# Performance work log

Hardware: AMD Instinct MI355X
Metric: run time of the kernel (lower is better)

Reference implementation:

```python
import jax, jax.numpy as jnp
import numpy as np

COMMITMENT_COST = 0.25

def setup_inputs() -> dict:
    key = jax.random.key(0)
    k1, k2 = jax.random.split(key)
    inputs = jax.random.normal(k1, (32, 64, 64, 64), dtype=jnp.float32)  # NCHW, C == embedding_dim
    num_embeddings, embedding_dim = 512, 64
    # nn.Embedding weight init: uniform(-1/num_embeddings, 1/num_embeddings)
    weight = jax.random.uniform(k2, (num_embeddings, embedding_dim), dtype=jnp.float32,
                                minval=-1.0 / num_embeddings, maxval=1.0 / num_embeddings)
    return {"inputs": inputs, "weight": weight}

def reference(inputs, weight):
    B, C, H, W = inputs.shape
    K, D = weight.shape
    # permute to NHWC then flatten tokens: [B*H*W, D]
    flat = jnp.transpose(inputs, (0, 2, 3, 1)).reshape(-1, D)
    # squared L2 distances to each codebook vector: [N, K]
    distances = (jnp.sum(flat * flat, axis=1, keepdims=True)
                 - 2.0 * flat @ weight.T
                 + jnp.sum(weight * weight, axis=1))
    encoding_indices = jnp.argmin(distances, axis=1)  # [N]
    # direct gather instead of one-hot matmul (same math)
    # NOTE: original code views flat (NHWC-ordered) rows back into the NCHW
    # input shape WITHOUT inverse-permuting -- replicated faithfully here.
    quantized = weight[encoding_indices].reshape(inputs.shape)
    e_latent_loss = jnp.mean((jax.lax.stop_gradient(quantized) - inputs) ** 2)
    q_latent_loss = jnp.mean((quantized - jax.lax.stop_gradient(inputs)) ** 2)
    loss = q_latent_loss + COMMITMENT_COST * e_latent_loss
    # straight-through estimator
    quantized_st = inputs + jax.lax.stop_gradient(quantized - inputs)
    # perplexity via index counts (equivalent to mean of one-hot encodings)
    N = flat.shape[0]
    counts = jnp.zeros((K,), dtype=flat.dtype).at[encoding_indices].add(1.0)
    avg_probs = counts / N
    perplexity = jnp.exp(-jnp.sum(avg_probs * jnp.log(avg_probs + 1e-10)))
    return quantized_st, loss, perplexity
```

## Files before the change

kernel.cpp:

```cpp
#include <hip/hip_runtime.h>
#include <math.h>


#define NTOK 131072
#define KCODES 512
#define HW 4096
#define CHW 262144
#define NELEM 8388608

typedef __attribute__((ext_vector_type(8))) short short8;
typedef __attribute__((ext_vector_type(4))) float f32x4;

static __device__ __forceinline__ unsigned short f2bf(float f) {
    unsigned u = __float_as_uint(f);
    unsigned r = u + 0x7FFFu + ((u >> 16) & 1u);
    return (unsigned short)(r >> 16);
}

__global__ __launch_bounds__(512, 4) void vq_main(const float* __restrict__ in,
                                                  const float* __restrict__ w,
                                                  float* __restrict__ out,
                                                  float* __restrict__ pcounts,
                                                  double* __restrict__ ssep,
                                                  float* __restrict__ counts,
                                                  double* __restrict__ sse_acc,
                                                  const int amode) {
    __shared__ unsigned short wh[KCODES * 64];
    __shared__ float wsqp[KCODES];
    __shared__ int idxbuf[256];
    __shared__ int hist[KCODES];
    __shared__ double sred[8];

    const int tid = threadIdx.x;
    const int lane = tid & 63, wv = tid >> 6;
    const int col = lane & 15, quad = lane >> 4;
    const int ntok0 = blockIdx.x * 256;

    wsqp[tid] = 1.25f;
    hist[tid] = 0;
    __syncthreads();

    const float* gbase = in + (ntok0 >> 12) * CHW + (ntok0 & 4095) + wv * 32 + col;
    short8 ah[2][2];
    float xsq = 0.f;
#pragma unroll
    for (int it = 0; it < 8; ++it) {
        const int g = it * 512 + tid;
        const int cc = g & 15, qd = (g >> 4) & 3, ch = (g >> 6) & 1, tt = g >> 7;
        const float4* src = (const float4*)(w + (tt * 16 + cc) * 64 + ch * 32 + qd * 8);
        const float4 v0 = src[0], v1 = src[1];
        const int sub = it >> 2, c = (it >> 1) & 1, j0 = (it & 1) * 4;
        const float* gp = gbase + sub * 16 + (c * 32 + quad * 8 + j0) * HW;
        const float x0 = gp[0 * HW], x1 = gp[1 * HW], x2 = gp[2 * HW], x3 = gp[3 * HW];

        short8 hv;
        hv[0] = (short)f2bf(v0.x); hv[1] = (short)f2bf(v0.y);
        hv[2] = (short)f2bf(v0.z); hv[3] = (short)f2bf(v0.w);
        hv[4] = (short)f2bf(v1.x); hv[5] = (short)f2bf(v1.y);
        hv[6] = (short)f2bf(v1.z); hv[7] = (short)f2bf(v1.w);
        *(short8*)(wh + g * 8) = hv;
        float ws2 = v0.x * v0.x;
        ws2 = fmaf(v0.y, v0.y, ws2); ws2 = fmaf(v0.z, v0.z, ws2);
        ws2 = fmaf(v0.w, v0.w, ws2); ws2 = fmaf(v1.x, v1.x, ws2);
        ws2 = fmaf(v1.y, v1.y, ws2); ws2 = fmaf(v1.z, v1.z, ws2);
        ws2 = fmaf(v1.w, v1.w, ws2);
        atomicAdd(&wsqp[tt * 16 + cc], ws2);

        ah[sub][c][j0 + 0] = (short)f2bf(-2.0f * x0);
        ah[sub][c][j0 + 1] = (short)f2bf(-2.0f * x1);
        ah[sub][c][j0 + 2] = (short)f2bf(-2.0f * x2);
        ah[sub][c][j0 + 3] = (short)f2bf(-2.0f * x3);
        xsq = fmaf(x0, x0, xsq); xsq = fmaf(x1, x1, xsq);
        xsq = fmaf(x2, x2, xsq); xsq = fmaf(x3, x3, xsq);
    }
    __syncthreads();

    unsigned runkey[2][4];
#pragma unroll
    for (int sub = 0; sub < 2; ++sub)
#pragma unroll
        for (int r = 0; r < 4; ++r) runkey[sub][r] = 0xFFFFFFFFu;

#pragma unroll 1
    for (int t = 0; t < 32; ++t) {
        const unsigned short* ph = wh + t * 1024 + quad * 128 + col * 8;
        const short8 b0 = *(const short8*)ph;
        const short8 b1 = *(const short8*)(ph + 512);
        const int code = t * 16 + col;
        const float seed = wsqp[code];
#pragma unroll
        for (int sub = 0; sub < 2; ++sub) {
            f32x4 acc = {seed, seed, seed, seed};
            acc = __builtin_amdgcn_mfma_f32_16x16x32_bf16(ah[sub][0], b0, acc, 0, 0, 0);
            acc = __builtin_amdgcn_mfma_f32_16x16x32_bf16(ah[sub][1], b1, acc, 0, 0, 0);
#pragma unroll
            for (int r = 0; r < 4; ++r) {
                const unsigned key = (__float_as_uint(acc[r]) << 9) | code;
                runkey[sub][r] = key < runkey[sub][r] ? key : runkey[sub][r];
            }
        }
    }

#pragma unroll
    for (int s = 1; s < 16; s <<= 1)
#pragma unroll
        for (int sub = 0; sub < 2; ++sub)
#pragma unroll
            for (int r = 0; r < 4; ++r) {
                const unsigned o = __shfl_xor(runkey[sub][r], s, 64);
                runkey[sub][r] = o < runkey[sub][r] ? o : runkey[sub][r];
            }

    float dsum = 0.f;
    if (col == 0) {
#pragma unroll
        for (int sub = 0; sub < 2; ++sub)
#pragma unroll
            for (int r = 0; r < 4; ++r) {
                const unsigned key = runkey[sub][r];
                idxbuf[wv * 32 + sub * 16 + quad * 4 + r] = (int)(key & 511u);
                dsum += __uint_as_float((key >> 9) | 0x3F800000u) - 1.25f;
            }
    }
    float contrib = xsq + dsum;
#pragma unroll
    for (int off = 32; off > 0; off >>= 1) contrib += __shfl_down(contrib, off, 64);
    if (lane == 0) sred[wv] = (double)contrib;
    __syncthreads();

    if (tid < 256) atomicAdd(&hist[idxbuf[tid]], 1);

#pragma unroll
    for (int p = 0; p < 2; ++p) {
        const int tl = p * 16 + (lane >> 2), q = lane & 3;
        const int n = ntok0 + wv * 32 + tl;
        const int bidx = idxbuf[wv * 32 + tl];
        const float4* wr = (const float4*)(w + bidx * 64 + q * 16);
        float4* op = (float4*)(out + n * 64 + q * 16);
#pragma unroll
        for (int i = 0; i < 4; ++i) op[i] = wr[i];
    }
    __syncthreads();

    if (!amode) {
        pcounts[(blockIdx.x << 9) + tid] = (float)hist[tid];
        if (tid == 0) {
            double s = sred[0];
#pragma unroll
            for (int i = 1; i < 8; ++i) s += sred[i];
            ssep[blockIdx.x] = s;
        }
    } else {
        const int h = hist[tid];
        if (h) atomicAdd(&counts[tid], (float)h);
        if (tid == 0) {
            double s = sred[0];
#pragma unroll
            for (int i = 1; i < 8; ++i) s += sred[i];
            atomicAdd(sse_acc, s);
        }
    }
}

__global__ __launch_bounds__(512) void vq_final_p(const float* __restrict__ pcounts,
                                                  const double* __restrict__ ssep,
                                                  float* __restrict__ out) {
    __shared__ float part[4][512];
    __shared__ double red[512];
    __shared__ double sred[512];
    const int t = threadIdx.x;
    const int q = t >> 7, c4 = (t & 127) << 2;

    const float4* base = (const float4*)pcounts + (q << 14) + (c4 >> 2);
    float4 s = {0.f, 0.f, 0.f, 0.f};
#pragma unroll 16
    for (int b = 0; b < 128; ++b) {
        const float4 v = base[b << 7];
        s.x += v.x; s.y += v.y; s.z += v.z; s.w += v.w;
    }
    *(float4*)&part[q][c4] = s;
    sred[t] = ssep[t];
    __syncthreads();

    const float cnt = part[0][t] + part[1][t] + part[2][t] + part[3][t];
    const double p = (double)cnt / (double)NTOK;
    red[t] = p * log(p + 1e-10);
    __syncthreads();
#pragma unroll
    for (int st = 256; st > 0; st >>= 1) {
        if (t < st) { red[t] += red[t + st]; sred[t] += sred[t + st]; }
        __syncthreads();
    }
    if (t == 0) {
        out[NELEM] = (float)((sred[0] / (double)NELEM) * 1.25);
        out[NELEM + 1] = (float)exp(-red[0]);
    }
}

__global__ __launch_bounds__(512) void vq_final_a(const float* __restrict__ counts,
                                                  const double* __restrict__ sse_acc,
                                                  float* __restrict__ out) {
    __shared__ double red[512];
    const int k = threadIdx.x;
    const double p = (double)counts[k] / (double)NTOK;
    red[k] = p * log(p + 1e-10);
    __syncthreads();
#pragma unroll
    for (int st = 256; st > 0; st >>= 1) {
        if (k < st) red[k] += red[k + st];
        __syncthreads();
    }
    if (k == 0) {
        out[NELEM] = (float)((*sse_acc / (double)NELEM) * 1.25);
        out[NELEM + 1] = (float)exp(-red[0]);
    }
}

extern "C" void kernel_launch(void* const* d_in, const int* in_sizes, int n_in,
                              void* d_out, int out_size, void* d_ws, size_t ws_size,
                              hipStream_t stream) {
    const float* in = (const float*)d_in[0];
    const float* w = (const float*)d_in[1];
    float* out = (float*)d_out;
    char* ws = (char*)d_ws;

    const size_t need = (size_t)512 * 512 * 4 + 512 * 8;
    if (ws_size >= need) {
        float* pcounts = (float*)ws;
        double* ssep = (double*)(ws + (size_t)512 * 512 * 4);
        vq_main<<<512, 512, 0, stream>>>(in, w, out, pcounts, ssep,
                                         nullptr, nullptr, 0);
        vq_final_p<<<1, 512, 0, stream>>>(pcounts, ssep, out);
    } else {
        float* counts = (float*)ws;
        double* sse_acc = (double*)(ws + 2048);
        hipMemsetAsync(ws, 0, 2056, stream);
        vq_main<<<512, 512, 0, stream>>>(in, w, out, nullptr, nullptr,
                                         counts, sse_acc, 1);
        vq_final_a<<<1, 512, 0, stream>>>(counts, sse_acc, out);
    }
}
```

Baseline: 117.4 us.

## Fuse final reduction into main kernel via last-block counters and nontemporal stores

Drops the separate final reduction kernel. Each block takes a ticket from a global atomic counter, and the last 16 blocks spin until all 512 blocks have finished. Those 16 then reduce slices of the per-block histograms, and a second counter picks one block to compute loss and perplexity. The histogram atomics also no longer wait on a block barrier, and the quantized output is written with nontemporal stores. This saves a kernel launch and the tail serialization, but adds a memset of the counters and spin-waiting that relies on all blocks being co-resident or otherwise making progress.

New measurement: 172.1 us. +46.6%, slower.

```diff
diff --git a/kernel.cpp b/kernel.cpp
--- a/kernel.cpp
+++ b/kernel.cpp
@@ -22,14 +22,17 @@
                                                   float* __restrict__ out,
                                                   float* __restrict__ pcounts,
                                                   double* __restrict__ ssep,
+                                                  float* __restrict__ part2,
+                                                  unsigned* __restrict__ ctrs,
                                                   float* __restrict__ counts,
                                                   double* __restrict__ sse_acc,
                                                   const int amode) {
-    __shared__ unsigned short wh[KCODES * 64];
+    __shared__ __align__(16) unsigned short wh[KCODES * 64];
     __shared__ float wsqp[KCODES];
     __shared__ int idxbuf[256];
     __shared__ int hist[KCODES];
     __shared__ double sred[8];
+    __shared__ int role_sh;
 
     const int tid = threadIdx.x;
     const int lane = tid & 63, wv = tid >> 6;
@@ -126,19 +129,21 @@
 #pragma unroll
     for (int off = 32; off > 0; off >>= 1) contrib += __shfl_down(contrib, off, 64);
     if (lane == 0) sred[wv] = (double)contrib;
-    __syncthreads();
-
-    if (tid < 256) atomicAdd(&hist[idxbuf[tid]], 1);
+
+    if (lane < 32) atomicAdd(&hist[idxbuf[wv * 32 + lane]], 1);
 
 #pragma unroll
     for (int p = 0; p < 2; ++p) {
         const int tl = p * 16 + (lane >> 2), q = lane & 3;
         const int n = ntok0 + wv * 32 + tl;
         const int bidx = idxbuf[wv * 32 + tl];
-        const float4* wr = (const float4*)(w + bidx * 64 + q * 16);
-        float4* op = (float4*)(out + n * 64 + q * 16);
-#pragma unroll
-        for (int i = 0; i < 4; ++i) op[i] = wr[i];
+        const f32x4* wr = (const f32x4*)(w + bidx * 64 + q * 16);
+        f32x4* op = (f32x4*)(out + n * 64 + q * 16);
+#pragma unroll
+        for (int i = 0; i < 4; ++i) {
+            const f32x4 v = wr[i];
+            __builtin_nontemporal_store(v, op + i);
+        }
     }
     __syncthreads();
 
@@ -149,6 +154,61 @@
 #pragma unroll
             for (int i = 1; i < 8; ++i) s += sred[i];
             ssep[blockIdx.x] = s;
+        }
+        __syncthreads();
+        if (tid == 0) {
+            __threadfence();
+            role_sh = (int)atomicAdd(ctrs, 1u);
+        }
+        __syncthreads();
+        const int old = role_sh;
+
+        if (old >= 512 - 16) {
+            const int r = old - (512 - 16);
+            if (tid == 0) {
+                while (__hip_atomic_load(ctrs, __ATOMIC_RELAXED,
+                                         __HIP_MEMORY_SCOPE_AGENT) < 512u)
+                    __builtin_amdgcn_s_sleep(2);
+            }
+            __syncthreads();
+            __threadfence();
+
+            const float* pc = pcounts + (r << 14) + tid;
+            float s = 0.f;
+#pragma unroll
+            for (int b = 0; b < 32; ++b) s += pc[b << 9];
+            part2[(r << 9) + tid] = s;
+            __syncthreads();
+            if (tid == 0) {
+                __threadfence();
+                role_sh = (int)atomicAdd(ctrs + 1, 1u);
+            }
+            __syncthreads();
+
+            if (role_sh == 15) {
+                __threadfence();
+                double* const dred = (double*)wh;
+                double* const dsred = dred + KCODES;
+                float cnt = 0.f;
+#pragma unroll
+                for (int rr = 0; rr < 16; ++rr) cnt += part2[(rr << 9) + tid];
+                const double p = (double)cnt / (double)NTOK;
+                dred[tid] = p * log(p + 1e-10);
+                dsred[tid] = ssep[tid];
+                __syncthreads();
+#pragma unroll
+                for (int st = 256; st > 0; st >>= 1) {
+                    if (tid < st) {
+                        dred[tid] += dred[tid + st];
+                        dsred[tid] += dsred[tid + st];
+                    }
+                    __syncthreads();
+                }
+                if (tid == 0) {
+                    out[NELEM] = (float)((dsred[0] / (double)NELEM) * 1.25);
+                    out[NELEM + 1] = (float)exp(-dred[0]);
+                }
+            }
         }
     } else {
         const int h = hist[tid];
@@ -159,41 +219,6 @@
             for (int i = 1; i < 8; ++i) s += sred[i];
             atomicAdd(sse_acc, s);
         }
-    }
-}
-
-__global__ __launch_bounds__(512) void vq_final_p(const float* __restrict__ pcounts,
-                                                  const double* __restrict__ ssep,
-                                                  float* __restrict__ out) {
-    __shared__ float part[4][512];
-    __shared__ double red[512];
-    __shared__ double sred[512];
-    const int t = threadIdx.x;
-    const int q = t >> 7, c4 = (t & 127) << 2;
-
-    const float4* base = (const float4*)pcounts + (q << 14) + (c4 >> 2);
-    float4 s = {0.f, 0.f, 0.f, 0.f};
-#pragma unroll 16
-    for (int b = 0; b < 128; ++b) {
-        const float4 v = base[b << 7];
-        s.x += v.x; s.y += v.y; s.z += v.z; s.w += v.w;
-    }
-    *(float4*)&part[q][c4] = s;
-    sred[t] = ssep[t];
-    __syncthreads();
-
-    const float cnt = part[0][t] + part[1][t] + part[2][t] + part[3][t];
-    const double p = (double)cnt / (double)NTOK;
-    red[t] = p * log(p + 1e-10);
-    __syncthreads();
-#pragma unroll
-    for (int st = 256; st > 0; st >>= 1) {
-        if (t < st) { red[t] += red[t + st]; sred[t] += sred[t + st]; }
-        __syncthreads();
-    }
-    if (t == 0) {
-        out[NELEM] = (float)((sred[0] / (double)NELEM) * 1.25);
-        out[NELEM + 1] = (float)exp(-red[0]);
     }
 }
 
@@ -224,19 +249,25 @@
     float* out = (float*)d_out;
     char* ws = (char*)d_ws;
 
-    const size_t need = (size_t)512 * 512 * 4 + 512 * 8;
+    const size_t PC = 0;
+    const size_t SS = (size_t)1 << 20;
+    const size_t P2 = SS + 4096;
+    const size_t CT = P2 + 32768;
+    const size_t need = CT + 8;
     if (ws_size >= need) {
-        float* pcounts = (float*)ws;
-        double* ssep = (double*)(ws + (size_t)512 * 512 * 4);
-        vq_main<<<512, 512, 0, stream>>>(in, w, out, pcounts, ssep,
+        float* pcounts = (float*)(ws + PC);
+        double* ssep = (double*)(ws + SS);
+        float* part2 = (float*)(ws + P2);
+        unsigned* ctrs = (unsigned*)(ws + CT);
+        (void)hipMemsetAsync(ctrs, 0, 8, stream);
+        vq_main<<<512, 512, 0, stream>>>(in, w, out, pcounts, ssep, part2, ctrs,
                                          nullptr, nullptr, 0);
-        vq_final_p<<<1, 512, 0, stream>>>(pcounts, ssep, out);
     } else {
         float* counts = (float*)ws;
         double* sse_acc = (double*)(ws + 2048);
-        hipMemsetAsync(ws, 0, 2056, stream);
-        vq_main<<<512, 512, 0, stream>>>(in, w, out, nullptr, nullptr,
-                                         counts, sse_acc, 1);
+        (void)hipMemsetAsync(ws, 0, 2056, stream);
+        vq_main<<<512, 512, 0, stream>>>(in, w, out, nullptr, nullptr, nullptr,
+                                         nullptr, counts, sse_acc, 1);
         vq_final_a<<<1, 512, 0, stream>>>(counts, sse_acc, out);
     }
 }
```

## Halve per-block tokens, stage codebook in two LDS halves, use byte partial counts

Applied to the files above, without the earlier changes.

Each block now handles 128 tokens instead of 256, launching 1024 blocks, and the bf16 codebook is staged through LDS in two 256-code halves. This halves LDS use (32KB to 16KB) and register state per block, allowing a higher occupancy hint of 8 waves-per-EU, so more blocks run concurrently to hide input-load latency. The trade is an extra barrier and a second conversion pass per block, and each block converts the codebook on twice as many blocks overall. Per-block histograms are written as bytes and unpacked in the final kernel, shrinking partial-count traffic, and the final reduction now sums two SSE partials per thread.

After: 126.6 us. 1.08x slower.

```diff
diff --git a/kernel.cpp b/kernel.cpp
--- a/kernel.cpp
+++ b/kernel.cpp
@@ -17,40 +17,41 @@
     return (unsigned short)(r >> 16);
 }
 
-__global__ __launch_bounds__(512, 4) void vq_main(const float* __restrict__ in,
+__global__ __launch_bounds__(512, 8) void vq_main(const float* __restrict__ in,
                                                   const float* __restrict__ w,
                                                   float* __restrict__ out,
-                                                  float* __restrict__ pcounts,
+                                                  unsigned char* __restrict__ pcounts,
                                                   double* __restrict__ ssep,
                                                   float* __restrict__ counts,
                                                   double* __restrict__ sse_acc,
                                                   const int amode) {
-    __shared__ unsigned short wh[KCODES * 64];
+    __shared__ __align__(16) unsigned short wh[256 * 64];
     __shared__ float wsqp[KCODES];
-    __shared__ int idxbuf[256];
+    __shared__ int idxbuf[128];
     __shared__ int hist[KCODES];
     __shared__ double sred[8];
 
     const int tid = threadIdx.x;
     const int lane = tid & 63, wv = tid >> 6;
     const int col = lane & 15, quad = lane >> 4;
-    const int ntok0 = blockIdx.x * 256;
+    const int ntok0 = blockIdx.x * 128;
 
     wsqp[tid] = 1.25f;
     hist[tid] = 0;
     __syncthreads();
 
-    const float* gbase = in + (ntok0 >> 12) * CHW + (ntok0 & 4095) + wv * 32 + col;
-    short8 ah[2][2];
+    const float* gbase = in + (ntok0 >> 12) * CHW + (ntok0 & 4095) + wv * 16 + col;
+    short8 ah[2];
     float xsq = 0.f;
 #pragma unroll
-    for (int it = 0; it < 8; ++it) {
+    for (int it = 0; it < 4; ++it) {
         const int g = it * 512 + tid;
         const int cc = g & 15, qd = (g >> 4) & 3, ch = (g >> 6) & 1, tt = g >> 7;
-        const float4* src = (const float4*)(w + (tt * 16 + cc) * 64 + ch * 32 + qd * 8);
+        const int code = tt * 16 + cc;
+        const float4* src = (const float4*)(w + code * 64 + ch * 32 + qd * 8);
         const float4 v0 = src[0], v1 = src[1];
-        const int sub = it >> 2, c = (it >> 1) & 1, j0 = (it & 1) * 4;
-        const float* gp = gbase + sub * 16 + (c * 32 + quad * 8 + j0) * HW;
+        const int c = it >> 1, j0 = (it & 1) * 4;
+        const float* gp = gbase + (c * 32 + quad * 8 + j0) * HW;
         const float x0 = gp[0 * HW], x1 = gp[1 * HW], x2 = gp[2 * HW], x3 = gp[3 * HW];
 
         short8 hv;
@@ -64,77 +65,106 @@
         ws2 = fmaf(v0.w, v0.w, ws2); ws2 = fmaf(v1.x, v1.x, ws2);
         ws2 = fmaf(v1.y, v1.y, ws2); ws2 = fmaf(v1.z, v1.z, ws2);
         ws2 = fmaf(v1.w, v1.w, ws2);
-        atomicAdd(&wsqp[tt * 16 + cc], ws2);
-
-        ah[sub][c][j0 + 0] = (short)f2bf(-2.0f * x0);
-        ah[sub][c][j0 + 1] = (short)f2bf(-2.0f * x1);
-        ah[sub][c][j0 + 2] = (short)f2bf(-2.0f * x2);
-        ah[sub][c][j0 + 3] = (short)f2bf(-2.0f * x3);
+        atomicAdd(&wsqp[code], ws2);
+
+        ah[c][j0 + 0] = (short)f2bf(-2.0f * x0);
+        ah[c][j0 + 1] = (short)f2bf(-2.0f * x1);
+        ah[c][j0 + 2] = (short)f2bf(-2.0f * x2);
+        ah[c][j0 + 3] = (short)f2bf(-2.0f * x3);
         xsq = fmaf(x0, x0, xsq); xsq = fmaf(x1, x1, xsq);
         xsq = fmaf(x2, x2, xsq); xsq = fmaf(x3, x3, xsq);
     }
     __syncthreads();
 
-    unsigned runkey[2][4];
-#pragma unroll
-    for (int sub = 0; sub < 2; ++sub)
-#pragma unroll
-        for (int r = 0; r < 4; ++r) runkey[sub][r] = 0xFFFFFFFFu;
+    unsigned runkey[4];
+#pragma unroll
+    for (int r = 0; r < 4; ++r) runkey[r] = 0xFFFFFFFFu;
 
 #pragma unroll 1
-    for (int t = 0; t < 32; ++t) {
+    for (int t = 0; t < 16; ++t) {
         const unsigned short* ph = wh + t * 1024 + quad * 128 + col * 8;
         const short8 b0 = *(const short8*)ph;
         const short8 b1 = *(const short8*)(ph + 512);
         const int code = t * 16 + col;
         const float seed = wsqp[code];
-#pragma unroll
-        for (int sub = 0; sub < 2; ++sub) {
-            f32x4 acc = {seed, seed, seed, seed};
-            acc = __builtin_amdgcn_mfma_f32_16x16x32_bf16(ah[sub][0], b0, acc, 0, 0, 0);
-            acc = __builtin_amdgcn_mfma_f32_16x16x32_bf16(ah[sub][1], b1, acc, 0, 0, 0);
-#pragma unroll
-            for (int r = 0; r < 4; ++r) {
-                const unsigned key = (__float_as_uint(acc[r]) << 9) | code;
-                runkey[sub][r] = key < runkey[sub][r] ? key : runkey[sub][r];
-            }
+        f32x4 acc = {seed, seed, seed, seed};
+        acc = __builtin_amdgcn_mfma_f32_16x16x32_bf16(ah[0], b0, acc, 0, 0, 0);
+        acc = __builtin_amdgcn_mfma_f32_16x16x32_bf16(ah[1], b1, acc, 0, 0, 0);
+#pragma unroll
+        for (int r = 0; r < 4; ++r) {
+            const unsigned key = (__float_as_uint(acc[r]) << 9) | code;
+            runkey[r] = key < runkey[r] ? key : runkey[r];
+        }
+    }
+    __syncthreads();
+
+#pragma unroll
+    for (int it = 0; it < 4; ++it) {
+        const int g = it * 512 + tid;
+        const int cc = g & 15, qd = (g >> 4) & 3, ch = (g >> 6) & 1, tt = g >> 7;
+        const int code = 256 + tt * 16 + cc;
+        const float4* src = (const float4*)(w + code * 64 + ch * 32 + qd * 8);
+        const float4 v0 = src[0], v1 = src[1];
+        short8 hv;
+        hv[0] = (short)f2bf(v0.x); hv[1] = (short)f2bf(v0.y);
+        hv[2] = (short)f2bf(v0.z); hv[3] = (short)f2bf(v0.w);
+        hv[4] = (short)f2bf(v1.x); hv[5] = (short)f2bf(v1.y);
+        hv[6] = (short)f2bf(v1.z); hv[7] = (short)f2bf(v1.w);
+        *(short8*)(wh + g * 8) = hv;
+        float ws2 = v0.x * v0.x;
+        ws2 = fmaf(v0.y, v0.y, ws2); ws2 = fmaf(v0.z, v0.z, ws2);
+        ws2 = fmaf(v0.w, v0.w, ws2); ws2 = fmaf(v1.x, v1.x, ws2);
+        ws2 = fmaf(v1.y, v1.y, ws2); ws2 = fmaf(v1.z, v1.z, ws2);
+        ws2 = fmaf(v1.w, v1.w, ws2);
+        atomicAdd(&wsqp[code], ws2);
+    }
+    __syncthreads();
+
+#pragma unroll 1
+    for (int t = 0; t < 16; ++t) {
+        const unsigned short* ph = wh + t * 1024 + quad * 128 + col * 8;
+        const short8 b0 = *(const short8*)ph;
+        const short8 b1 = *(const short8*)(ph + 512);
+        const int code = 256 + t * 16 + col;
+        const float seed = wsqp[code];
+        f32x4 acc = {seed, seed, seed, seed};
+        acc = __builtin_amdgcn_mfma_f32_16x16x32_bf16(ah[0], b0, acc, 0, 0, 0);
+        acc = __builtin_amdgcn_mfma_f32_16x16x32_bf16(ah[1], b1, acc, 0, 0, 0);
+#pragma unroll
+        for (int r = 0; r < 4; ++r) {
+            const unsigned key = (__float_as_uint(acc[r]) << 9) | code;
+            runkey[r] = key < runkey[r] ? key : runkey[r];
         }
     }
 
 #pragma unroll
     for (int s = 1; s < 16; s <<= 1)
 #pragma unroll
-        for (int sub = 0; sub < 2; ++sub)
-#pragma unroll
-            for (int r = 0; r < 4; ++r) {
-                const unsigned o = __shfl_xor(runkey[sub][r], s, 64);
-                runkey[sub][r] = o < runkey[sub][r] ? o : runkey[sub][r];
-            }
+        for (int r = 0; r < 4; ++r) {
+            const unsigned o = __shfl_xor(runkey[r], s, 64);
+            runkey[r] = o < runkey[r] ? o : runkey[r];
+        }
 
     float dsum = 0.f;
     if (col == 0) {
 #pragma unroll
-        for (int sub = 0; sub < 2; ++sub)
-#pragma unroll
-            for (int r = 0; r < 4; ++r) {
-                const unsigned key = runkey[sub][r];
-                idxbuf[wv * 32 + sub * 16 + quad * 4 + r] = (int)(key & 511u);
-                dsum += __uint_as_float((key >> 9) | 0x3F800000u) - 1.25f;
-            }
+        for (int r = 0; r < 4; ++r) {
+            const unsigned key = runkey[r];
+            idxbuf[wv * 16 + quad * 4 + r] = (int)(key & 511u);
+            dsum += __uint_as_float((key >> 9) | 0x3F800000u) - 1.25f;
+        }
     }
     float contrib = xsq + dsum;
 #pragma unroll
     for (int off = 32; off > 0; off >>= 1) contrib += __shfl_down(contrib, off, 64);
     if (lane == 0) sred[wv] = (double)contrib;
-    __syncthreads();
-
-    if (tid < 256) atomicAdd(&hist[idxbuf[tid]], 1);
-
-#pragma unroll
-    for (int p = 0; p < 2; ++p) {
-        const int tl = p * 16 + (lane >> 2), q = lane & 3;
-        const int n = ntok0 + wv * 32 + tl;
-        const int bidx = idxbuf[wv * 32 + tl];
+
+    if (lane < 16) atomicAdd(&hist[idxbuf[wv * 16 + lane]], 1);
+
+    {
+        const int tl = lane >> 2, q = lane & 3;
+        const int n = ntok0 + wv * 16 + tl;
+        const int bidx = idxbuf[wv * 16 + tl];
         const float4* wr = (const float4*)(w + bidx * 64 + q * 16);
         float4* op = (float4*)(out + n * 64 + q * 16);
 #pragma unroll
@@ -143,7 +173,7 @@
     __syncthreads();
 
     if (!amode) {
-        pcounts[(blockIdx.x << 9) + tid] = (float)hist[tid];
+        pcounts[(blockIdx.x << 9) + tid] = (unsigned char)hist[tid];
         if (tid == 0) {
             double s = sred[0];
 #pragma unroll
@@ -162,27 +192,29 @@
     }
 }
 
-__global__ __launch_bounds__(512) void vq_final_p(const float* __restrict__ pcounts,
+__global__ __launch_bounds__(512) void vq_final_p(const unsigned char* __restrict__ pcounts,
                                                   const double* __restrict__ ssep,
                                                   float* __restrict__ out) {
-    __shared__ float part[4][512];
+    __shared__ unsigned part[4][512];
     __shared__ double red[512];
     __shared__ double sred[512];
     const int t = threadIdx.x;
     const int q = t >> 7, c4 = (t & 127) << 2;
 
-    const float4* base = (const float4*)pcounts + (q << 14) + (c4 >> 2);
-    float4 s = {0.f, 0.f, 0.f, 0.f};
+    const unsigned* base = (const unsigned*)(pcounts + (size_t)(q << 8) * 512 + c4);
+    unsigned s0 = 0, s1 = 0, s2 = 0, s3 = 0;
 #pragma unroll 16
-    for (int b = 0; b < 128; ++b) {
-        const float4 v = base[b << 7];
-        s.x += v.x; s.y += v.y; s.z += v.z; s.w += v.w;
-    }
-    *(float4*)&part[q][c4] = s;
-    sred[t] = ssep[t];
-    __syncthreads();
-
-    const float cnt = part[0][t] + part[1][t] + part[2][t] + part[3][t];
+    for (int b = 0; b < 256; ++b) {
+        const unsigned v = base[b << 7];
+        s0 += v & 255u; s1 += (v >> 8) & 255u;
+        s2 += (v >> 16) & 255u; s3 += v >> 24;
+    }
+    part[q][c4] = s0; part[q][c4 + 1] = s1;
+    part[q][c4 + 2] = s2; part[q][c4 + 3] = s3;
+    sred[t] = ssep[t] + ssep[t + 512];
+    __syncthreads();
+
+    const float cnt = (float)(part[0][t] + part[1][t] + part[2][t] + part[3][t]);
     const double p = (double)cnt / (double)NTOK;
     red[t] = p * log(p + 1e-10);
     __syncthreads();
@@ -224,19 +256,20 @@
     float* out = (float*)d_out;
     char* ws = (char*)d_ws;
 
-    const size_t need = (size_t)512 * 512 * 4 + 512 * 8;
+    const size_t SS = (size_t)1024 * 512;
+    const size_t need = SS + 1024 * 8;
     if (ws_size >= need) {
-        float* pcounts = (float*)ws;
-        double* ssep = (double*)(ws + (size_t)512 * 512 * 4);
-        vq_main<<<512, 512, 0, stream>>>(in, w, out, pcounts, ssep,
-                                         nullptr, nullptr, 0);
+        unsigned char* pcounts = (unsigned char*)ws;
+        double* ssep = (double*)(ws + SS);
+        vq_main<<<1024, 512, 0, stream>>>(in, w, out, pcounts, ssep,
+                                          nullptr, nullptr, 0);
         vq_final_p<<<1, 512, 0, stream>>>(pcounts, ssep, out);
     } else {
         float* counts = (float*)ws;
         double* sse_acc = (double*)(ws + 2048);
-        hipMemsetAsync(ws, 0, 2056, stream);
-        vq_main<<<512, 512, 0, stream>>>(in, w, out, nullptr, nullptr,
-                                         counts, sse_acc, 1);
+        (void)hipMemsetAsync(ws, 0, 2056, stream);
+        vq_main<<<1024, 512, 0, stream>>>(in, w, out, nullptr, nullptr,
+                                          counts, sse_acc, 1);
         vq_final_a<<<1, 512, 0, stream>>>(counts, sse_acc, out);
     }
 }
```

## Halve codebook LDS by two-pass chunking, raise occupancy, shrink partial counts

Applied to the files above, without the earlier changes.

The bf16 codebook staging in shared memory is cut from 512 to 256 codes. The kernel scans the first half, syncs, reloads the second half into the same buffer, then scans again. This halves LDS use so the launch bound can ask for 8 waves per SIMD instead of 4, raising occupancy to hide global load latency, at the cost of an extra barrier, a second weight reload phase and tighter register limits. Per-block histogram partials are stored as uint16 instead of float to cut workspace traffic, and one block-wide barrier before the histogram atomics is removed by having each wave count its own tokens.

Result: no change. 116.5 us (-0.8%).

```diff
diff --git a/kernel.cpp b/kernel.cpp
--- a/kernel.cpp
+++ b/kernel.cpp
@@ -10,6 +10,7 @@
 
 typedef __attribute__((ext_vector_type(8))) short short8;
 typedef __attribute__((ext_vector_type(4))) float f32x4;
+typedef __attribute__((ext_vector_type(4))) unsigned short u16x4;
 
 static __device__ __forceinline__ unsigned short f2bf(float f) {
     unsigned u = __float_as_uint(f);
@@ -17,15 +18,15 @@
     return (unsigned short)(r >> 16);
 }
 
-__global__ __launch_bounds__(512, 4) void vq_main(const float* __restrict__ in,
+__global__ __launch_bounds__(512, 8) void vq_main(const float* __restrict__ in,
                                                   const float* __restrict__ w,
                                                   float* __restrict__ out,
-                                                  float* __restrict__ pcounts,
+                                                  unsigned short* __restrict__ pcounts,
                                                   double* __restrict__ ssep,
                                                   float* __restrict__ counts,
                                                   double* __restrict__ sse_acc,
                                                   const int amode) {
-    __shared__ unsigned short wh[KCODES * 64];
+    __shared__ __align__(16) unsigned short wh[256 * 64];
     __shared__ float wsqp[KCODES];
     __shared__ int idxbuf[256];
     __shared__ int hist[KCODES];
@@ -45,14 +46,73 @@
     float xsq = 0.f;
 #pragma unroll
     for (int it = 0; it < 8; ++it) {
-        const int g = it * 512 + tid;
-        const int cc = g & 15, qd = (g >> 4) & 3, ch = (g >> 6) & 1, tt = g >> 7;
-        const float4* src = (const float4*)(w + (tt * 16 + cc) * 64 + ch * 32 + qd * 8);
-        const float4 v0 = src[0], v1 = src[1];
         const int sub = it >> 2, c = (it >> 1) & 1, j0 = (it & 1) * 4;
         const float* gp = gbase + sub * 16 + (c * 32 + quad * 8 + j0) * HW;
         const float x0 = gp[0 * HW], x1 = gp[1 * HW], x2 = gp[2 * HW], x3 = gp[3 * HW];
 
+        if (it < 4) {
+            const int g = it * 512 + tid;
+            const int cc = g & 15, qd = (g >> 4) & 3, ch = (g >> 6) & 1, tt = g >> 7;
+            const int code = tt * 16 + cc;
+            const float4* src = (const float4*)(w + code * 64 + ch * 32 + qd * 8);
+            const float4 v0 = src[0], v1 = src[1];
+            short8 hv;
+            hv[0] = (short)f2bf(v0.x); hv[1] = (short)f2bf(v0.y);
+            hv[2] = (short)f2bf(v0.z); hv[3] = (short)f2bf(v0.w);
+            hv[4] = (short)f2bf(v1.x); hv[5] = (short)f2bf(v1.y);
+            hv[6] = (short)f2bf(v1.z); hv[7] = (short)f2bf(v1.w);
+            *(short8*)(wh + g * 8) = hv;
+            float ws2 = v0.x * v0.x;
+            ws2 = fmaf(v0.y, v0.y, ws2); ws2 = fmaf(v0.z, v0.z, ws2);
+            ws2 = fmaf(v0.w, v0.w, ws2); ws2 = fmaf(v1.x, v1.x, ws2);
+            ws2 = fmaf(v1.y, v1.y, ws2); ws2 = fmaf(v1.z, v1.z, ws2);
+            ws2 = fmaf(v1.w, v1.w, ws2);
+            atomicAdd(&wsqp[code], ws2);
+        }
+
+        ah[sub][c][j0 + 0] = (short)f2bf(-2.0f * x0);
+        ah[sub][c][j0 + 1] = (short)f2bf(-2.0f * x1);
+        ah[sub][c][j0 + 2] = (short)f2bf(-2.0f * x2);
+        ah[sub][c][j0 + 3] = (short)f2bf(-2.0f * x3);
+        xsq = fmaf(x0, x0, xsq); xsq = fmaf(x1, x1, xsq);
+        xsq = fmaf(x2, x2, xsq); xsq = fmaf(x3, x3, xsq);
+    }
+    __syncthreads();
+
+    unsigned runkey[2][4];
+#pragma unroll
+    for (int sub = 0; sub < 2; ++sub)
+#pragma unroll
+        for (int r = 0; r < 4; ++r) runkey[sub][r] = 0xFFFFFFFFu;
+
+#pragma unroll 1
+    for (int t = 0; t < 16; ++t) {
+        const unsigned short* ph = wh + t * 1024 + quad * 128 + col * 8;
+        const short8 b0 = *(const short8*)ph;
+        const short8 b1 = *(const short8*)(ph + 512);
+        const int code = t * 16 + col;
+        const float seed = wsqp[code];
+#pragma unroll
+        for (int sub = 0; sub < 2; ++sub) {
+            f32x4 acc = {seed, seed, seed, seed};
+            acc = __builtin_amdgcn_mfma_f32_16x16x32_bf16(ah[sub][0], b0, acc, 0, 0, 0);
+            acc = __builtin_amdgcn_mfma_f32_16x16x32_bf16(ah[sub][1], b1, acc, 0, 0, 0);
+#pragma unroll
+            for (int r = 0; r < 4; ++r) {
+                const unsigned key = (__float_as_uint(acc[r]) << 9) | code;
+                runkey[sub][r] = key < runkey[sub][r] ? key : runkey[sub][r];
+            }
+        }
+    }
+    __syncthreads();
+
+#pragma unroll
+    for (int it = 0; it < 4; ++it) {
+        const int g = it * 512 + tid;
+        const int cc = g & 15, qd = (g >> 4) & 3, ch = (g >> 6) & 1, tt = g >> 7;
+        const int code = 256 + tt * 16 + cc;
+        const float4* src = (const float4*)(w + code * 64 + ch * 32 + qd * 8);
+        const float4 v0 = src[0], v1 = src[1];
         short8 hv;
         hv[0] = (short)f2bf(v0.x); hv[1] = (short)f2bf(v0.y);
         hv[2] = (short)f2bf(v0.z); hv[3] = (short)f2bf(v0.w);
@@ -64,29 +124,16 @@
         ws2 = fmaf(v0.w, v0.w, ws2); ws2 = fmaf(v1.x, v1.x, ws2);
         ws2 = fmaf(v1.y, v1.y, ws2); ws2 = fmaf(v1.z, v1.z, ws2);
         ws2 = fmaf(v1.w, v1.w, ws2);
-        atomicAdd(&wsqp[tt * 16 + cc], ws2);
-
-        ah[sub][c][j0 + 0] = (short)f2bf(-2.0f * x0);
-        ah[sub][c][j0 + 1] = (short)f2bf(-2.0f * x1);
-        ah[sub][c][j0 + 2] = (short)f2bf(-2.0f * x2);
-        ah[sub][c][j0 + 3] = (short)f2bf(-2.0f * x3);
-        xsq = fmaf(x0, x0, xsq); xsq = fmaf(x1, x1, xsq);
-        xsq = fmaf(x2, x2, xsq); xsq = fmaf(x3, x3, xsq);
-    }
-    __syncthreads();
-
-    unsigned runkey[2][4];
-#pragma unroll
-    for (int sub = 0; sub < 2; ++sub)
-#pragma unroll
-        for (int r = 0; r < 4; ++r) runkey[sub][r] = 0xFFFFFFFFu;
+        atomicAdd(&wsqp[code], ws2);
+    }
+    __syncthreads();
 
 #pragma unroll 1
-    for (int t = 0; t < 32; ++t) {
+    for (int t = 0; t < 16; ++t) {
         const unsigned short* ph = wh + t * 1024 + quad * 128 + col * 8;
         const short8 b0 = *(const short8*)ph;
         const short8 b1 = *(const short8*)(ph + 512);
-        const int code = t * 16 + col;
+        const int code = 256 + t * 16 + col;
         const float seed = wsqp[code];
 #pragma unroll
         for (int sub = 0; sub < 2; ++sub) {
@@ -126,9 +173,8 @@
 #pragma unroll
     for (int off = 32; off > 0; off >>= 1) contrib += __shfl_down(contrib, off, 64);
     if (lane == 0) sred[wv] = (double)contrib;
-    __syncthreads();
-
-    if (tid < 256) atomicAdd(&hist[idxbuf[tid]], 1);
+
+    if (lane < 32) atomicAdd(&hist[idxbuf[wv * 32 + lane]], 1);
 
 #pragma unroll
     for (int p = 0; p < 2; ++p) {
@@ -143,7 +189,7 @@
     __syncthreads();
 
     if (!amode) {
-        pcounts[(blockIdx.x << 9) + tid] = (float)hist[tid];
+        pcounts[(blockIdx.x << 9) + tid] = (unsigned short)hist[tid];
         if (tid == 0) {
             double s = sred[0];
 #pragma unroll
@@ -162,7 +208,7 @@
     }
 }
 
-__global__ __launch_bounds__(512) void vq_final_p(const float* __restrict__ pcounts,
+__global__ __launch_bounds__(512) void vq_final_p(const unsigned short* __restrict__ pcounts,
                                                   const double* __restrict__ ssep,
                                                   float* __restrict__ out) {
     __shared__ float part[4][512];
@@ -171,12 +217,13 @@
     const int t = threadIdx.x;
     const int q = t >> 7, c4 = (t & 127) << 2;
 
-    const float4* base = (const float4*)pcounts + (q << 14) + (c4 >> 2);
+    const u16x4* base = (const u16x4*)pcounts + (q << 14) + (c4 >> 2);
     float4 s = {0.f, 0.f, 0.f, 0.f};
 #pragma unroll 16
     for (int b = 0; b < 128; ++b) {
-        const float4 v = base[b << 7];
-        s.x += v.x; s.y += v.y; s.z += v.z; s.w += v.w;
+        const u16x4 v = base[b << 7];
+        s.x += (float)v[0]; s.y += (float)v[1];
+        s.z += (float)v[2]; s.w += (float)v[3];
     }
     *(float4*)&part[q][c4] = s;
     sred[t] = ssep[t];
@@ -224,17 +271,18 @@
     float* out = (float*)d_out;
     char* ws = (char*)d_ws;
 
-    const size_t need = (size_t)512 * 512 * 4 + 512 * 8;
+    const size_t SS = (size_t)512 * 512 * 2;
+    const size_t need = SS + 512 * 8;
     if (ws_size >= need) {
-        float* pcounts = (float*)ws;
-        double* ssep = (double*)(ws + (size_t)512 * 512 * 4);
+        unsigned short* pcounts = (unsigned short*)ws;
+        double* ssep = (double*)(ws + SS);
         vq_main<<<512, 512, 0, stream>>>(in, w, out, pcounts, ssep,
                                          nullptr, nullptr, 0);
         vq_final_p<<<1, 512, 0, stream>>>(pcounts, ssep, out);
     } else {
         float* counts = (float*)ws;
         double* sse_acc = (double*)(ws + 2048);
-        hipMemsetAsync(ws, 0, 2056, stream);
+        (void)hipMemsetAsync(ws, 0, 2056, stream);
         vq_main<<<512, 512, 0, stream>>>(in, w, out, nullptr, nullptr,
                                          counts, sse_acc, 1);
         vq_final_a<<<1, 512, 0, stream>>>(counts, sse_acc, out);
```
